# Kernel optimization log

Measured on AMD Instinct MI355X. Metric: run time of the kernel, lower is better.

Reference implementation:

```python
import jax, jax.numpy as jnp
import numpy as np

VOCAB = 32000
D_MODEL = 192
N_LAYERS = 8
D_STATE = 64
EXPAND = 2
D_CONV = 3
NUM_CLASSES = 2
D_INNER = EXPAND * D_MODEL            # 384
DT_RANK = (D_MODEL + 15) // 16        # 12 (mamba_ssm default ceil(d_model/16))
EPS = 1e-6


def rmsnorm(x, w):
    return w * x * jax.lax.rsqrt(jnp.mean(x * x, axis=-1, keepdims=True) + EPS)


def selective_scan(u, dt, A, Bm, Cm):
    # u, dt: (b, T, d_inner); Bm, Cm: (b, T, d_state); A: (d_inner, d_state)
    def step(h, xs):
        dt_t, B_t, C_t, u_t = xs                      # (b,di),(b,ds),(b,ds),(b,di)
        dA = jnp.exp(dt_t[:, :, None] * A)            # (b, di, ds)
        h = dA * h + (dt_t * u_t)[:, :, None] * B_t[:, None, :]
        y = jnp.einsum('bdn,bn->bd', h, C_t)
        return h, y

    b = u.shape[0]
    h0 = jnp.zeros((b, D_INNER, D_STATE), u.dtype)
    xs = (jnp.swapaxes(dt, 0, 1), jnp.swapaxes(Bm, 0, 1),
          jnp.swapaxes(Cm, 0, 1), jnp.swapaxes(u, 0, 1))
    _, ys = jax.lax.scan(step, h0, xs)                # ys: (T, b, di)
    return jnp.swapaxes(ys, 0, 1)


def mamba_layer(x, p):
    # one residual Mamba block: x + Mamba(RMSNorm(x))
    norm_w, in_w, cw, cb, xpw, dtw, dtb, Alog, Dp, ow = p
    h = rmsnorm(x, norm_w)
    xz = jnp.einsum('btd,ed->bte', h, in_w)           # (b, T, 2*di)
    xi, z = jnp.split(xz, 2, axis=-1)
    # causal depthwise conv over time
    xc = jnp.swapaxes(xi, 1, 2)                       # (b, di, T)
    xc = jax.lax.conv_general_dilated(xc, cw[:, None, :], (1,),
                                      [(D_CONV - 1, 0)],
                                      feature_group_count=D_INNER)
    xi = jax.nn.silu(jnp.swapaxes(xc, 1, 2) + cb)
    dbl = jnp.einsum('btc,ec->bte', xi, xpw)          # (b, T, dt_rank+2*ds)
    dt_r = dbl[..., :DT_RANK]
    Bm = dbl[..., DT_RANK:DT_RANK + D_STATE]
    Cm = dbl[..., DT_RANK + D_STATE:]
    dt = jax.nn.softplus(jnp.einsum('btr,dr->btd', dt_r, dtw) + dtb)
    A = -jnp.exp(Alog)
    y = selective_scan(xi, dt, A, Bm, Cm) + xi * Dp
    y = y * jax.nn.silu(z)
    return x + jnp.einsum('bte,de->btd', y, ow)


def setup_inputs():
    key = jax.random.key(0)
    ks = jax.random.split(key, 12)
    B, L = 8, 1024
    s = 0.02
    input_ids = jax.random.randint(ks[0], (B, L), 0, VOCAB, dtype=jnp.int32)
    attention_mask = jnp.ones((B, L), dtype=jnp.int32)
    embed = jax.random.normal(ks[1], (VOCAB, D_MODEL), jnp.float32) * s
    cls = jax.random.normal(ks[2], (1, 1, D_MODEL), jnp.float32) * s
    norm_w = jnp.ones((N_LAYERS, D_MODEL), jnp.float32)
    in_proj_w = jax.random.normal(ks[3], (N_LAYERS, 2 * D_INNER, D_MODEL), jnp.float32) * s
    conv_w = jax.random.normal(ks[4], (N_LAYERS, D_INNER, D_CONV), jnp.float32) * s
    conv_b = jnp.zeros((N_LAYERS, D_INNER), jnp.float32)
    x_proj_w = jax.random.normal(ks[5], (N_LAYERS, DT_RANK + 2 * D_STATE, D_INNER), jnp.float32) * s
    dt_proj_w = jax.random.normal(ks[6], (N_LAYERS, D_INNER, DT_RANK), jnp.float32) * s
    dt_proj_b = jnp.zeros((N_LAYERS, D_INNER), jnp.float32)
    # mamba_ssm S4D-real init: A_log = log(1..d_state)
    A_log = jnp.log(jnp.tile(jnp.arange(1.0, D_STATE + 1, dtype=jnp.float32)[None, None, :],
                             (N_LAYERS, D_INNER, 1)))
    D_param = jnp.ones((N_LAYERS, D_INNER), jnp.float32)
    out_proj_w = jax.random.normal(ks[7], (N_LAYERS, D_MODEL, D_INNER), jnp.float32) * s
    final_norm_w = jnp.ones((D_MODEL,), jnp.float32)
    head_w = embed[:NUM_CLASSES]            # tie_embeddings=True
    head_b = jnp.zeros((NUM_CLASSES,), jnp.float32)
    return dict(input_ids=input_ids, attention_mask=attention_mask, embed=embed,
                cls=cls, norm_w=norm_w, in_proj_w=in_proj_w, conv_w=conv_w,
                conv_b=conv_b, x_proj_w=x_proj_w, dt_proj_w=dt_proj_w,
                dt_proj_b=dt_proj_b, A_log=A_log, D_param=D_param,
                out_proj_w=out_proj_w, final_norm_w=final_norm_w,
                head_w=head_w, head_b=head_b)


def reference(input_ids, attention_mask, embed, cls, norm_w, in_proj_w, conv_w,
              conv_b, x_proj_w, dt_proj_w, dt_proj_b, A_log, D_param,
              out_proj_w, final_norm_w, head_w, head_b):
    x = embed[input_ids]                               # (b, L, d)
    b = x.shape[0]
    x = jnp.concatenate([x, jnp.broadcast_to(cls, (b, 1, D_MODEL))], axis=1)
    layer_fn = jax.checkpoint(mamba_layer)

    def body(x, p):
        return layer_fn(x, p), None

    x, _ = jax.lax.scan(body, x, (norm_w, in_proj_w, conv_w, conv_b, x_proj_w,
                                  dt_proj_w, dt_proj_b, A_log, D_param, out_proj_w))
    x = rmsnorm(x, final_norm_w)
    m = attention_mask.astype(x.dtype)                 # (b, L)
    denom = jnp.clip(jnp.sum(m, axis=1, keepdims=True), 1.0, None)
    pooled = jnp.sum(x[:, :-1] * m[..., None], axis=1) / denom
    return pooled @ head_w.T + head_b                  # (b, num_classes)
```

## Files before the change

kernel.cpp:

```cpp
#include <hip/hip_runtime.h>
#include <hip/hip_bf16.h>
#include <cstddef>

namespace {

constexpr int NB   = 8;
constexpr int LSEQ = 1025;
constexpr int TSEQ = 1024;
constexpr int DM   = 192;
constexpr int DI   = 384;
constexpr int DXZ  = 768;
constexpr int DBLW = 140;
constexpr int DTR  = 12;
constexpr int NST  = 64;
constexpr int MROWS = NB * LSEQ;
constexpr int NCH  = 32;
constexpr int CS   = 32;
constexpr int NCH1 = NCH - 1;
constexpr int NDG  = DI / 64;
constexpr int HST  = 32;
constexpr int XPAD = 144;
constexpr float LOG2E = 1.4426950408889634f;

using bf16x8 = __attribute__((ext_vector_type(8))) short;
using f32x4  = __attribute__((ext_vector_type(4))) float;

__device__ __forceinline__ float waveReduceSum(float v) {
#pragma unroll
  for (int o = 32; o; o >>= 1) v += __shfl_xor(v, o, 64);
  return v;
}

__device__ __forceinline__ unsigned short f2bf(float v) {
  __hip_bfloat16 b = __float2bfloat16(v);
  return *reinterpret_cast<unsigned short*>(&b);
}

__global__ void embed_kernel(const int* __restrict__ ids, const float* __restrict__ emb,
                             const float* __restrict__ cls, float* __restrict__ x) {
  int idx = blockIdx.x * blockDim.x + threadIdx.x;
  if (idx >= NB * LSEQ * DM) return;
  int d = idx % DM;
  int bt = idx / DM;
  int t = bt % LSEQ, b = bt / LSEQ;
  float v;
  if (t < TSEQ) v = emb[(size_t)ids[b * TSEQ + t] * DM + d];
  else          v = cls[d];
  x[idx] = v;
}

__global__ void cvt_bf16_kernel(const float* __restrict__ src, unsigned short* __restrict__ dst,
                                int n) {
  int idx = blockIdx.x * blockDim.x + threadIdx.x;
  if (idx < n) dst[idx] = f2bf(src[idx]);
}

__global__ void pad_xp_kernel(const float* __restrict__ src, unsigned short* __restrict__ dst) {
  int idx = blockIdx.x * blockDim.x + threadIdx.x;
  if (idx >= 8 * XPAD * DI) return;
  int k = idx % DI;
  int n = (idx / DI) % XPAD;
  int l = idx / (DI * XPAD);
  float v = (n < DBLW) ? src[((size_t)l * DBLW + n) * DI + k] : 0.f;
  dst[idx] = f2bf(v);
}

__global__ void transpose_batched(const float* __restrict__ in, float* __restrict__ out,
                                  int rows, int cols) {
  __shared__ float tile[32][33];
  int l = blockIdx.z;
  int r0 = blockIdx.y * 32, c0 = blockIdx.x * 32;
  const float* src = in + (size_t)l * rows * cols;
  float* dst = out + (size_t)l * rows * cols;
  int tx = threadIdx.x, ty = threadIdx.y;
#pragma unroll
  for (int i = 0; i < 32; i += 8) {
    int r = r0 + ty + i, c = c0 + tx;
    if (r < rows && c < cols) tile[ty + i][tx] = src[(size_t)r * cols + c];
  }
  __syncthreads();
#pragma unroll
  for (int i = 0; i < 32; i += 8) {
    int c = c0 + ty + i, r = r0 + tx;
    if (c < cols && r < rows) dst[(size_t)c * rows + r] = tile[tx][ty + i];
  }
}

__global__ __launch_bounds__(192)
void rmsnorm_kernel(const float* __restrict__ x, const float* __restrict__ w,
                    unsigned short* __restrict__ h) {
  int row = blockIdx.x;
  int d = threadIdx.x;
  float v = x[(size_t)row * DM + d];
  float ss = waveReduceSum(v * v);
  __shared__ float red[3];
  if ((d & 63) == 0) red[d >> 6] = ss;
  __syncthreads();
  float ms = (red[0] + red[1] + red[2]) * (1.f / DM);
  h[(size_t)row * DM + d] = f2bf(v * rsqrtf(ms + 1e-6f) * w[d]);
}

template <int EPI, int ASRC>
__global__ __launch_bounds__(256)
void gemm_mfma(const unsigned short* __restrict__ A, const float* __restrict__ A0,
               const float* __restrict__ A1, const unsigned short* __restrict__ W,
               float* __restrict__ C, int M, int Nw, int Nstore, int K, int ldc) {
  __shared__ unsigned short Alds[128][40];
  __shared__ unsigned short Wlds[64][40];
  const int tid = threadIdx.x;
  const int w = tid >> 6, lane = tid & 63;
  const int r16 = lane & 15, g = lane >> 4;
  const int row0 = blockIdx.y * 128, col0 = blockIdx.x * 64;

  f32x4 acc[2][4];
#pragma unroll
  for (int mi = 0; mi < 2; ++mi)
#pragma unroll
    for (int ni = 0; ni < 4; ++ni) acc[mi][ni] = (f32x4){0.f, 0.f, 0.f, 0.f};

  for (int k0 = 0; k0 < K; k0 += 32) {
#pragma unroll
    for (int cc = 0; cc < 2; ++cc) {
      int c = tid + cc * 256;
      int r = c >> 2, q = c & 3;
      uint4 v = make_uint4(0, 0, 0, 0);
      int grow = row0 + r;
      if (grow < M) {
        if (ASRC == 0) {
          v = *(const uint4*)(A + (size_t)grow * K + k0 + q * 8);
        } else {
          const float* s0 = A0 + (size_t)grow * K + k0 + q * 8;
          const float* s1 = A1 + (size_t)grow * K + k0 + q * 8;
          float4 p0 = *(const float4*)s0, p1 = *(const float4*)(s0 + 4);
          float4 q0 = *(const float4*)s1, q1 = *(const float4*)(s1 + 4);
          v.x = (unsigned)f2bf(p0.x + q0.x) | ((unsigned)f2bf(p0.y + q0.y) << 16);
          v.y = (unsigned)f2bf(p0.z + q0.z) | ((unsigned)f2bf(p0.w + q0.w) << 16);
          v.z = (unsigned)f2bf(p1.x + q1.x) | ((unsigned)f2bf(p1.y + q1.y) << 16);
          v.w = (unsigned)f2bf(p1.z + q1.z) | ((unsigned)f2bf(p1.w + q1.w) << 16);
        }
      }
      *(uint4*)&Alds[r][q * 8] = v;
    }
    {
      int r = tid >> 2, q = tid & 3;
      uint4 v = make_uint4(0, 0, 0, 0);
      int gn = col0 + r;
      if (gn < Nw) v = *(const uint4*)(W + (size_t)gn * K + k0 + q * 8);
      *(uint4*)&Wlds[r][q * 8] = v;
    }
    __syncthreads();
    bf16x8 a_f[2], b_f[4];
#pragma unroll
    for (int mi = 0; mi < 2; ++mi)
      a_f[mi] = *(const bf16x8*)&Alds[w * 32 + mi * 16 + r16][g * 8];
#pragma unroll
    for (int ni = 0; ni < 4; ++ni)
      b_f[ni] = *(const bf16x8*)&Wlds[ni * 16 + r16][g * 8];
#pragma unroll
    for (int mi = 0; mi < 2; ++mi)
#pragma unroll
      for (int ni = 0; ni < 4; ++ni)
        acc[mi][ni] = __builtin_amdgcn_mfma_f32_16x16x32_bf16(a_f[mi], b_f[ni],
                                                              acc[mi][ni], 0, 0, 0);
    __syncthreads();
  }
#pragma unroll
  for (int mi = 0; mi < 2; ++mi) {
#pragma unroll
    for (int reg = 0; reg < 4; ++reg) {
      int row = row0 + w * 32 + mi * 16 + g * 4 + reg;
      if (row >= M) continue;
#pragma unroll
      for (int ni = 0; ni < 4; ++ni) {
        int col = col0 + ni * 16 + r16;
        if (col >= Nstore) continue;
        size_t idx = (size_t)row * ldc + col;
        if (EPI) C[idx] += acc[mi][ni][reg];
        else     C[idx] = acc[mi][ni][reg];
      }
    }
  }
}

__global__ void conv_kernel(const float* __restrict__ xz, const float* __restrict__ cw,
                            const float* __restrict__ cb, float* __restrict__ xi,
                            unsigned short* __restrict__ xi16, float* __restrict__ zg) {
  int idx = blockIdx.x * blockDim.x + threadIdx.x;
  if (idx >= NB * LSEQ * DI) return;
  int c = idx % DI;
  int bt = idx / DI;
  int t = bt % LSEQ, b = bt / LSEQ;
  const float* src = xz + (size_t)b * LSEQ * DXZ + c;
  float s = cb[c];
  float w0 = cw[c * 3 + 0], w1 = cw[c * 3 + 1], w2 = cw[c * 3 + 2];
  if (t >= 2) s = fmaf(w0, src[(size_t)(t - 2) * DXZ], s);
  if (t >= 1) s = fmaf(w1, src[(size_t)(t - 1) * DXZ], s);
  s = fmaf(w2, src[(size_t)t * DXZ], s);
  float sig = 1.f / (1.f + __expf(-s));
  float u = s * sig;
  xi[idx] = u;
  xi16[idx] = f2bf(u);
  float zv = src[(size_t)t * DXZ + DI];
  float zsig = 1.f / (1.f + __expf(-zv));
  zg[idx] = zv * zsig;
}

__global__ __launch_bounds__(384)
void dt_kernel(const float* __restrict__ dbl, const float* __restrict__ dtwT,
               const float* __restrict__ dtb, float* __restrict__ dtout) {
  int row0 = blockIdx.x * 4;
  int d = threadIdx.x;
  __shared__ float rr[4][DTR];
  if (d < 4 * DTR) rr[d / DTR][d % DTR] = dbl[(size_t)(row0 + d / DTR) * DBLW + (d % DTR)];
  float w[DTR];
#pragma unroll
  for (int r = 0; r < DTR; ++r) w[r] = dtwT[r * DI + d];
  float bias = dtb[d];
  __syncthreads();
#pragma unroll
  for (int q = 0; q < 4; ++q) {
    float s = bias;
#pragma unroll
    for (int r = 0; r < DTR; ++r) s = fmaf(rr[q][r], w[r], s);
    float sp = fmaxf(s, 0.f) + log1pf(__expf(-fabsf(s)));
    dtout[(size_t)(row0 + q) * DI + d] = sp;
  }
}


__global__ __launch_bounds__(256, 3)
void scan_pass1(const float* __restrict__ dtp_, const float* __restrict__ xi,
                const float* __restrict__ dbl, const float* __restrict__ Alog,
                float* __restrict__ cumdt, float* __restrict__ H) {
  __shared__ float Bt[2][CS][64];
  const int tid = threadIdx.x;
  const int wid = tid >> 6, lane = tid & 63;
  const int q = wid >> 1, half = wid & 1;
  const int unit = blockIdx.x * 2 + q;
  const int c = unit % NCH1;
  const int bg = unit / NCH1;
  const int b = bg / NDG, dgrp = bg % NDG;
  const int d = dgrp * 64 + lane;
  const int n0 = half * HST;
  const int t0 = c * CS;

  {
    const float* srcB = dbl + ((size_t)b * LSEQ + t0) * DBLW + DTR + lane;
    for (int r = half; r < CS; r += 2) Bt[q][r][lane] = srcB[(size_t)r * DBLW];
  }

  const float* Ap = Alog + (size_t)d * NST;
  float a0 = __expf(Ap[0]);
  bool okl = true;
#pragma unroll
  for (int j = 0; j < HST; ++j) {
    float aj = __expf(Ap[n0 + j]);
    okl = okl && (fabsf(aj - (float)(n0 + j + 1) * a0) <= 1e-3f * (float)(n0 + j + 1) * fabsf(a0));
  }
  const bool fast = __all(okl);
  const float al2u = -a0 * LOG2E;

  float h[HST];
#pragma unroll
  for (int j = 0; j < HST; ++j) h[j] = 0.f;

  __syncthreads();

  const float* dtp = dtp_ + ((size_t)b * LSEQ + t0) * DI + d;
  const float* up  = xi   + ((size_t)b * LSEQ + t0) * DI + d;
  float cum = 0.f;
  float dtv = *dtp, uv = *up;

  if (fast) {
    for (int t = 0; t < CS; ++t) {
      float n_dt = 0.f, n_u = 0.f;
      if (t + 1 < CS) {
        dtp += DI; up += DI;
        n_dt = *dtp; n_u = *up;
      }
      float dtu = dtv * uv;
      float m = dtv * al2u;
      float r1 = exp2f(m);
      float p = (n0 == 0) ? r1 : exp2f(m * (float)(n0 + 1));
      float r2 = r1 * r1, r4 = r2 * r2;
      float s0 = p, s1 = p * r1, s2 = p * r2, s3 = s2 * r1;
#pragma unroll
      for (int k = 0; k < 8; ++k) {
        float4 B4 = *(const float4*)&Bt[q][t][n0 + 4 * k];
        h[4 * k + 0] = fmaf(s0, h[4 * k + 0], dtu * B4.x);
        h[4 * k + 1] = fmaf(s1, h[4 * k + 1], dtu * B4.y);
        h[4 * k + 2] = fmaf(s2, h[4 * k + 2], dtu * B4.z);
        h[4 * k + 3] = fmaf(s3, h[4 * k + 3], dtu * B4.w);
        if (k < 7) { s0 *= r4; s1 *= r4; s2 *= r4; s3 *= r4; }
      }
      cum += dtv;
      dtv = n_dt; uv = n_u;
    }
  } else {
    for (int t = 0; t < CS; ++t) {
      float n_dt = 0.f, n_u = 0.f;
      if (t + 1 < CS) {
        dtp += DI; up += DI;
        n_dt = *dtp; n_u = *up;
      }
      float dtu = dtv * uv;
      for (int j = 0; j < HST; ++j) {
        float aj = -__expf(Ap[n0 + j]) * LOG2E;
        h[j] = fmaf(exp2f(dtv * aj), h[j], dtu * Bt[q][t][n0 + j]);
      }
      cum += dtv;
      dtv = n_dt; uv = n_u;
    }
  }

  if (half == 0)
    cumdt[(size_t)bg * NCH1 * 64 + (size_t)c * 64 + lane] = cum;
  float* hp = H + ((size_t)bg * NCH + (c + 1)) * NST * 64 + (size_t)n0 * 64 + lane;
#pragma unroll
  for (int j = 0; j < HST; ++j) hp[j * 64] = h[j];
}

__global__ __launch_bounds__(256)
void scan_pass2(const float* __restrict__ cumdt, const float* __restrict__ Alog,
                float* __restrict__ H) {
  int gw = blockIdx.x * 4 + (threadIdx.x >> 6);
  int lane = threadIdx.x & 63;
  int bg = gw >> 4;
  int nq = (gw & 15) * 4;
  int dgrp = bg % NDG;
  int d = dgrp * 64 + lane;

  float al2[4];
#pragma unroll
  for (int j = 0; j < 4; ++j) al2[j] = -__expf(Alog[(size_t)d * NST + nq + j]) * LOG2E;

  float h[4] = {0.f, 0.f, 0.f, 0.f};

  float* H0 = H + ((size_t)bg * NCH) * NST * 64 + (size_t)nq * 64 + lane;
#pragma unroll
  for (int j = 0; j < 4; ++j) H0[j * 64] = 0.f;

  for (int c = 1; c < NCH; ++c) {
    float cum = cumdt[(size_t)bg * NCH1 * 64 + (size_t)(c - 1) * 64 + lane];
    float* Hc = H + ((size_t)bg * NCH + c) * NST * 64 + (size_t)nq * 64 + lane;
#pragma unroll
    for (int j = 0; j < 4; ++j) {
      float he = Hc[j * 64];
      h[j] = fmaf(exp2f(al2[j] * cum), h[j], he);
      Hc[j * 64] = h[j];
    }
  }
}

__global__ __launch_bounds__(256, 3)
void scan_pass3(const float* __restrict__ dtp_, const float* __restrict__ xi,
                const float* __restrict__ zg, const float* __restrict__ dbl,
                const float* __restrict__ Alog, const float* __restrict__ Dpar,
                const float* __restrict__ H, float* __restrict__ yg0,
                float* __restrict__ yg1) {
  __shared__ float Bt[2][CS + 1][64];
  __shared__ float Ct[2][CS + 1][64];
  const int tid = threadIdx.x;
  const int wid = tid >> 6, lane = tid & 63;
  const int q = wid >> 1, half = wid & 1;
  const int unit = blockIdx.x * 2 + q;
  const int c = unit & (NCH - 1);
  const int bg = unit >> 5;
  const int b = bg / NDG, dgrp = bg % NDG;
  const int d = dgrp * 64 + lane;
  const int n0 = half * HST;
  const int t0 = c * CS;
  const int nsteps = (c == NCH - 1) ? (LSEQ - t0) : CS;

  {
    const float* srcB = dbl + ((size_t)b * LSEQ + t0) * DBLW + DTR + (half ? NST : 0) + lane;
    float* dst = half ? &Ct[q][0][lane] : &Bt[q][0][lane];
    for (int r = 0; r < nsteps; ++r) dst[r * 64] = srcB[(size_t)r * DBLW];
  }

  const float* Ap = Alog + (size_t)d * NST;
  float a0 = __expf(Ap[0]);
  bool okl = true;
#pragma unroll
  for (int j = 0; j < HST; ++j) {
    float aj = __expf(Ap[n0 + j]);
    okl = okl && (fabsf(aj - (float)(n0 + j + 1) * a0) <= 1e-3f * (float)(n0 + j + 1) * fabsf(a0));
  }
  const bool fast = __all(okl);
  const float al2u = -a0 * LOG2E;

  float Dp = Dpar[d];
  float h[HST];
  {
    const float* hi = H + ((size_t)bg * NCH + c) * NST * 64 + (size_t)n0 * 64 + lane;
#pragma unroll
    for (int j = 0; j < HST; ++j) h[j] = hi[j * 64];
  }

  __syncthreads();

  const float* dtp = dtp_ + ((size_t)b * LSEQ + t0) * DI + d;
  const float* up  = xi   + ((size_t)b * LSEQ + t0) * DI + d;
  const float* gp  = zg   + ((size_t)b * LSEQ + t0) * DI + d;
  float* yp = (half == 0 ? yg0 : yg1) + ((size_t)b * LSEQ + t0) * DI + d;

  float dtv = *dtp, uv = *up, gv = *gp;

  if (fast) {
    for (int t = 0; t < nsteps; ++t) {
      float n_dt = 0.f, n_u = 0.f, n_g = 0.f;
      if (t + 1 < nsteps) {
        dtp += DI; up += DI; gp += DI;
        n_dt = *dtp; n_u = *up; n_g = *gp;
      }
      float dtu = dtv * uv;
      float m = dtv * al2u;
      float r1 = exp2f(m);
      float p = (n0 == 0) ? r1 : exp2f(m * (float)(n0 + 1));
      float r2 = r1 * r1, r4 = r2 * r2;
      float s0 = p, s1 = p * r1, s2 = p * r2, s3 = s2 * r1;
      float y = 0.f;
#pragma unroll
      for (int k = 0; k < 8; ++k) {
        float4 B4 = *(const float4*)&Bt[q][t][n0 + 4 * k];
        float4 C4 = *(const float4*)&Ct[q][t][n0 + 4 * k];
        h[4 * k + 0] = fmaf(s0, h[4 * k + 0], dtu * B4.x);
        y = fmaf(h[4 * k + 0], C4.x, y);
        h[4 * k + 1] = fmaf(s1, h[4 * k + 1], dtu * B4.y);
        y = fmaf(h[4 * k + 1], C4.y, y);
        h[4 * k + 2] = fmaf(s2, h[4 * k + 2], dtu * B4.z);
        y = fmaf(h[4 * k + 2], C4.z, y);
        h[4 * k + 3] = fmaf(s3, h[4 * k + 3], dtu * B4.w);
        y = fmaf(h[4 * k + 3], C4.w, y);
        if (k < 7) { s0 *= r4; s1 *= r4; s2 *= r4; s3 *= r4; }
      }
      float outv = (half == 0) ? fmaf(uv, Dp, y) * gv : y * gv;
      *yp = outv;
      yp += DI;
      dtv = n_dt; uv = n_u; gv = n_g;
    }
  } else {
    for (int t = 0; t < nsteps; ++t) {
      float n_dt = 0.f, n_u = 0.f, n_g = 0.f;
      if (t + 1 < nsteps) {
        dtp += DI; up += DI; gp += DI;
        n_dt = *dtp; n_u = *up; n_g = *gp;
      }
      float dtu = dtv * uv;
      float y = 0.f;
      for (int j = 0; j < HST; ++j) {
        float aj = -__expf(Ap[n0 + j]) * LOG2E;
        h[j] = fmaf(exp2f(dtv * aj), h[j], dtu * Bt[q][t][n0 + j]);
        y = fmaf(h[j], Ct[q][t][n0 + j], y);
      }
      float outv = (half == 0) ? fmaf(uv, Dp, y) * gv : y * gv;
      *yp = outv;
      yp += DI;
      dtv = n_dt; uv = n_u; gv = n_g;
    }
  }
}

__global__ __launch_bounds__(192)
void pool1_kernel(const float* __restrict__ x, const int* __restrict__ mask,
                  const float* __restrict__ fw, float* __restrict__ partial) {
  int b = blockIdx.x >> 6;
  int chunk = blockIdx.x & 63;
  int d = threadIdx.x;
  __shared__ float red[3];
  float w = fw[d];
  float acc = 0.f;
  for (int tt = 0; tt < 16; ++tt) {
    int t = chunk * 16 + tt;
    float v = x[((size_t)b * LSEQ + t) * DM + d];
    float ss = waveReduceSum(v * v);
    if ((d & 63) == 0) red[d >> 6] = ss;
    __syncthreads();
    float ms = (red[0] + red[1] + red[2]) * (1.f / DM);
    float m = (float)mask[b * TSEQ + t];
    acc = fmaf(v * rsqrtf(ms + 1e-6f) * w, m, acc);
    __syncthreads();
  }
  partial[((size_t)b * 64 + chunk) * DM + d] = acc;
}

__global__ __launch_bounds__(192)
void pool2_kernel(const float* __restrict__ partial, const int* __restrict__ mask,
                  const float* __restrict__ hw, const float* __restrict__ hb,
                  float* __restrict__ out) {
  int b = blockIdx.x;
  int d = threadIdx.x;
  float s = 0.f;
  for (int c = 0; c < 64; ++c) s += partial[((size_t)b * 64 + c) * DM + d];
  float den = 0.f;
  for (int t = d; t < TSEQ; t += DM) den += (float)mask[b * TSEQ + t];
  den = waveReduceSum(den);
  __shared__ float dred[3];
  __shared__ float pooled[DM];
  if ((d & 63) == 0) dred[d >> 6] = den;
  __syncthreads();
  float denom = fmaxf(dred[0] + dred[1] + dred[2], 1.f);
  pooled[d] = s / denom;
  __syncthreads();
  if (d < 2) {
    float acc = hb[d];
    for (int k = 0; k < DM; ++k) acc = fmaf(pooled[k], hw[d * DM + k], acc);
    out[b * 2 + d] = acc;
  }
}

}

extern "C" void kernel_launch(void* const* d_in, const int* in_sizes, int n_in,
                              void* d_out, int out_size, void* d_ws, size_t ws_size,
                              hipStream_t stream) {
  const int*   ids    = (const int*)d_in[0];
  const int*   mask   = (const int*)d_in[1];
  const float* embed  = (const float*)d_in[2];
  const float* cls    = (const float*)d_in[3];
  const float* norm_w = (const float*)d_in[4];
  const float* in_w   = (const float*)d_in[5];
  const float* conv_w = (const float*)d_in[6];
  const float* conv_b = (const float*)d_in[7];
  const float* xp_w   = (const float*)d_in[8];
  const float* dtw    = (const float*)d_in[9];
  const float* dtb    = (const float*)d_in[10];
  const float* Alog   = (const float*)d_in[11];
  const float* Dpar   = (const float*)d_in[12];
  const float* ow     = (const float*)d_in[13];
  const float* fnw    = (const float*)d_in[14];
  const float* hw     = (const float*)d_in[15];
  const float* hb     = (const float*)d_in[16];
  float* out = (float*)d_out;

  char* base = (char*)d_ws;
  size_t off = 0;
  auto alloc = [&](size_t bytes) -> void* {
    void* p = base + off;
    off = (off + bytes + 255) & ~(size_t)255;
    return p;
  };

  float* x      = (float*)alloc((size_t)NB * LSEQ * DM * 4);
  unsigned short* h16 = (unsigned short*)alloc((size_t)NB * LSEQ * DM * 2);
  float* xz     = (float*)alloc((size_t)NB * LSEQ * DXZ * 4);
  float* xi     = (float*)alloc((size_t)NB * LSEQ * DI * 4);
  unsigned short* xi16 = (unsigned short*)alloc((size_t)NB * LSEQ * DI * 2);
  float* zgbuf  = (float*)alloc((size_t)NB * LSEQ * DI * 4);
  float* dblb   = (float*)alloc((size_t)NB * LSEQ * DBLW * 4);
  float* dtbuf  = (float*)alloc((size_t)NB * LSEQ * DI * 4);
  float* yg0    = (float*)alloc((size_t)NB * LSEQ * DI * 4);
  float* yg1    = (float*)alloc((size_t)NB * LSEQ * DI * 4);
  unsigned short* wb_in = (unsigned short*)alloc((size_t)8 * DXZ * DM * 2);
  unsigned short* wb_xp = (unsigned short*)alloc((size_t)8 * XPAD * DI * 2);
  unsigned short* wb_ow = (unsigned short*)alloc((size_t)8 * DM * DI * 2);
  float* wT_dt  = (float*)alloc((size_t)8 * DTR * DI * 4);
  float* partial = (float*)alloc((size_t)NB * 64 * DM * 4);
  float* cumdt  = (float*)alloc((size_t)NB * NDG * NCH1 * 64 * 4);
  float* Hbuf   = (float*)alloc((size_t)NB * NDG * NCH * NST * 64 * 4);

  cvt_bf16_kernel<<<(8 * DXZ * DM + 255) / 256, 256, 0, stream>>>(in_w, wb_in, 8 * DXZ * DM);
  pad_xp_kernel<<<(8 * XPAD * DI + 255) / 256, 256, 0, stream>>>(xp_w, wb_xp);
  cvt_bf16_kernel<<<(8 * DM * DI + 255) / 256, 256, 0, stream>>>(ow, wb_ow, 8 * DM * DI);
  dim3 tb(32, 8);
  transpose_batched<<<dim3(1, 12, 8), tb, 0, stream>>>(dtw, wT_dt, DI, DTR);

  embed_kernel<<<(NB * LSEQ * DM) / 256, 256, 0, stream>>>(ids, embed, cls, x);

  const int mtiles = (MROWS + 127) / 128;
  for (int l = 0; l < 8; ++l) {
    rmsnorm_kernel<<<MROWS, 192, 0, stream>>>(x, norm_w + l * DM, h16);
    gemm_mfma<0, 0><<<dim3(DXZ / 64, mtiles), 256, 0, stream>>>(
        h16, nullptr, nullptr, wb_in + (size_t)l * DXZ * DM, xz, MROWS, DXZ, DXZ, DM, DXZ);
    conv_kernel<<<(NB * LSEQ * DI) / 256, 256, 0, stream>>>(
        xz, conv_w + l * DI * 3, conv_b + l * DI, xi, xi16, zgbuf);
    gemm_mfma<0, 0><<<dim3(XPAD / 64 + 1, mtiles), 256, 0, stream>>>(
        xi16, nullptr, nullptr, wb_xp + (size_t)l * XPAD * DI, dblb, MROWS, XPAD, DBLW, DI, DBLW);
    dt_kernel<<<MROWS / 4, DI, 0, stream>>>(dblb, wT_dt + l * DTR * DI, dtb + l * DI, dtbuf);
    scan_pass1<<<(NB * NDG * NCH1) / 2, 256, 0, stream>>>(
        dtbuf, xi, dblb, Alog + (size_t)l * DI * NST, cumdt, Hbuf);
    scan_pass2<<<(NB * NDG * 16) / 4, 256, 0, stream>>>(
        cumdt, Alog + (size_t)l * DI * NST, Hbuf);
    scan_pass3<<<(NB * NDG * NCH) / 2, 256, 0, stream>>>(
        dtbuf, xi, zgbuf, dblb, Alog + (size_t)l * DI * NST, Dpar + l * DI, Hbuf,
        yg0, yg1);
    gemm_mfma<1, 1><<<dim3(DM / 64, mtiles), 256, 0, stream>>>(
        nullptr, yg0, yg1, wb_ow + (size_t)l * DM * DI, x, MROWS, DM, DM, DI, DM);
  }

  pool1_kernel<<<NB * 64, 192, 0, stream>>>(x, mask, fnw, partial);
  pool2_kernel<<<NB, 192, 0, stream>>>(partial, mask, hw, hb, out);
}
```

Measured before the change: 1.265 ms.

## Store xz and scan outputs in bf16, widen scan blocks to share B/C tiles

The in_proj GEMM now writes xz as bf16, and the conv kernel reads it back as bf16. The scan pass3 outputs yg0/yg1 are also stored as bf16 and summed pairwise in bf16 before the out_proj GEMM. This cuts global memory traffic for these intermediates roughly in half. Scan pass1 and pass3 are regrouped into 768-thread blocks covering all six d-groups of one (batch, chunk), so the B/C tiles are loaded into LDS once per block instead of once per d-group. The risks are extra bf16 rounding error in the intermediates and lower occupancy from the larger blocks.

```diff
diff --git a/kernel.cpp b/kernel.cpp
--- a/kernel.cpp
+++ b/kernel.cpp
@@ -35,6 +35,14 @@
   __hip_bfloat16 b = __float2bfloat16(v);
   return *reinterpret_cast<unsigned short*>(&b);
 }
+__device__ __forceinline__ float bf2f(unsigned short u) {
+  return __uint_as_float(((unsigned)u) << 16);
+}
+__device__ __forceinline__ unsigned addpair_bf(unsigned a, unsigned b) {
+  float alo = __uint_as_float(a << 16), ahi = __uint_as_float(a & 0xffff0000u);
+  float blo = __uint_as_float(b << 16), bhi = __uint_as_float(b & 0xffff0000u);
+  return ((unsigned)f2bf(alo + blo)) | (((unsigned)f2bf(ahi + bhi)) << 16);
+}
 
 __global__ void embed_kernel(const int* __restrict__ ids, const float* __restrict__ emb,
                              const float* __restrict__ cls, float* __restrict__ x) {
@@ -102,9 +110,10 @@
 
 template <int EPI, int ASRC>
 __global__ __launch_bounds__(256)
-void gemm_mfma(const unsigned short* __restrict__ A, const float* __restrict__ A0,
-               const float* __restrict__ A1, const unsigned short* __restrict__ W,
-               float* __restrict__ C, int M, int Nw, int Nstore, int K, int ldc) {
+void gemm_mfma(const unsigned short* __restrict__ A, const unsigned short* __restrict__ Ab0,
+               const unsigned short* __restrict__ Ab1, const unsigned short* __restrict__ W,
+               float* __restrict__ C, unsigned short* __restrict__ Cb,
+               int M, int Nw, int Nstore, int K, int ldc) {
   __shared__ unsigned short Alds[128][40];
   __shared__ unsigned short Wlds[64][40];
   const int tid = threadIdx.x;
@@ -129,14 +138,12 @@
         if (ASRC == 0) {
           v = *(const uint4*)(A + (size_t)grow * K + k0 + q * 8);
         } else {
-          const float* s0 = A0 + (size_t)grow * K + k0 + q * 8;
-          const float* s1 = A1 + (size_t)grow * K + k0 + q * 8;
-          float4 p0 = *(const float4*)s0, p1 = *(const float4*)(s0 + 4);
-          float4 q0 = *(const float4*)s1, q1 = *(const float4*)(s1 + 4);
-          v.x = (unsigned)f2bf(p0.x + q0.x) | ((unsigned)f2bf(p0.y + q0.y) << 16);
-          v.y = (unsigned)f2bf(p0.z + q0.z) | ((unsigned)f2bf(p0.w + q0.w) << 16);
-          v.z = (unsigned)f2bf(p1.x + q1.x) | ((unsigned)f2bf(p1.y + q1.y) << 16);
-          v.w = (unsigned)f2bf(p1.z + q1.z) | ((unsigned)f2bf(p1.w + q1.w) << 16);
+          uint4 a = *(const uint4*)(Ab0 + (size_t)grow * K + k0 + q * 8);
+          uint4 b = *(const uint4*)(Ab1 + (size_t)grow * K + k0 + q * 8);
+          v.x = addpair_bf(a.x, b.x);
+          v.y = addpair_bf(a.y, b.y);
+          v.z = addpair_bf(a.z, b.z);
+          v.w = addpair_bf(a.w, b.w);
         }
       }
       *(uint4*)&Alds[r][q * 8] = v;
@@ -175,14 +182,15 @@
         int col = col0 + ni * 16 + r16;
         if (col >= Nstore) continue;
         size_t idx = (size_t)row * ldc + col;
-        if (EPI) C[idx] += acc[mi][ni][reg];
-        else     C[idx] = acc[mi][ni][reg];
-      }
-    }
-  }
-}
-
-__global__ void conv_kernel(const float* __restrict__ xz, const float* __restrict__ cw,
+        if (EPI == 1)      C[idx] += acc[mi][ni][reg];
+        else if (EPI == 0) C[idx] = acc[mi][ni][reg];
+        else               Cb[idx] = f2bf(acc[mi][ni][reg]);
+      }
+    }
+  }
+}
+
+__global__ void conv_kernel(const unsigned short* __restrict__ xz16, const float* __restrict__ cw,
                             const float* __restrict__ cb, float* __restrict__ xi,
                             unsigned short* __restrict__ xi16, float* __restrict__ zg) {
   int idx = blockIdx.x * blockDim.x + threadIdx.x;
@@ -190,17 +198,17 @@
   int c = idx % DI;
   int bt = idx / DI;
   int t = bt % LSEQ, b = bt / LSEQ;
-  const float* src = xz + (size_t)b * LSEQ * DXZ + c;
+  const unsigned short* src = xz16 + (size_t)b * LSEQ * DXZ + c;
   float s = cb[c];
   float w0 = cw[c * 3 + 0], w1 = cw[c * 3 + 1], w2 = cw[c * 3 + 2];
-  if (t >= 2) s = fmaf(w0, src[(size_t)(t - 2) * DXZ], s);
-  if (t >= 1) s = fmaf(w1, src[(size_t)(t - 1) * DXZ], s);
-  s = fmaf(w2, src[(size_t)t * DXZ], s);
+  if (t >= 2) s = fmaf(w0, bf2f(src[(size_t)(t - 2) * DXZ]), s);
+  if (t >= 1) s = fmaf(w1, bf2f(src[(size_t)(t - 1) * DXZ]), s);
+  s = fmaf(w2, bf2f(src[(size_t)t * DXZ]), s);
   float sig = 1.f / (1.f + __expf(-s));
   float u = s * sig;
   xi[idx] = u;
   xi16[idx] = f2bf(u);
-  float zv = src[(size_t)t * DXZ + DI];
+  float zv = bf2f(src[(size_t)t * DXZ + DI]);
   float zsig = 1.f / (1.f + __expf(-zv));
   zg[idx] = zv * zsig;
 }
@@ -228,25 +236,24 @@
 }
 
 
-__global__ __launch_bounds__(256, 3)
+__global__ __launch_bounds__(768, 3)
 void scan_pass1(const float* __restrict__ dtp_, const float* __restrict__ xi,
                 const float* __restrict__ dbl, const float* __restrict__ Alog,
                 float* __restrict__ cumdt, float* __restrict__ H) {
-  __shared__ float Bt[2][CS][64];
+  __shared__ float Bt[CS][64];
   const int tid = threadIdx.x;
-  const int wid = tid >> 6, lane = tid & 63;
-  const int q = wid >> 1, half = wid & 1;
-  const int unit = blockIdx.x * 2 + q;
-  const int c = unit % NCH1;
-  const int bg = unit / NCH1;
-  const int b = bg / NDG, dgrp = bg % NDG;
+  const int w = tid >> 6, lane = tid & 63;
+  const int dgrp = w >> 1, half = w & 1;
+  const int b = blockIdx.x / NCH1;
+  const int c = blockIdx.x % NCH1;
+  const int bg = b * NDG + dgrp;
   const int d = dgrp * 64 + lane;
   const int n0 = half * HST;
   const int t0 = c * CS;
 
   {
     const float* srcB = dbl + ((size_t)b * LSEQ + t0) * DBLW + DTR + lane;
-    for (int r = half; r < CS; r += 2) Bt[q][r][lane] = srcB[(size_t)r * DBLW];
+    for (int r = w; r < CS; r += 12) Bt[r][lane] = srcB[(size_t)r * DBLW];
   }
 
   const float* Ap = Alog + (size_t)d * NST;
@@ -286,7 +293,7 @@
       float s0 = p, s1 = p * r1, s2 = p * r2, s3 = s2 * r1;
 #pragma unroll
       for (int k = 0; k < 8; ++k) {
-        float4 B4 = *(const float4*)&Bt[q][t][n0 + 4 * k];
+        float4 B4 = *(const float4*)&Bt[t][n0 + 4 * k];
         h[4 * k + 0] = fmaf(s0, h[4 * k + 0], dtu * B4.x);
         h[4 * k + 1] = fmaf(s1, h[4 * k + 1], dtu * B4.y);
         h[4 * k + 2] = fmaf(s2, h[4 * k + 2], dtu * B4.z);
@@ -306,7 +313,7 @@
       float dtu = dtv * uv;
       for (int j = 0; j < HST; ++j) {
         float aj = -__expf(Ap[n0 + j]) * LOG2E;
-        h[j] = fmaf(exp2f(dtv * aj), h[j], dtu * Bt[q][t][n0 + j]);
+        h[j] = fmaf(exp2f(dtv * aj), h[j], dtu * Bt[t][n0 + j]);
       }
       cum += dtv;
       dtv = n_dt; uv = n_u;
@@ -352,30 +359,33 @@
   }
 }
 
-__global__ __launch_bounds__(256, 3)
+__global__ __launch_bounds__(768, 3)
 void scan_pass3(const float* __restrict__ dtp_, const float* __restrict__ xi,
                 const float* __restrict__ zg, const float* __restrict__ dbl,
                 const float* __restrict__ Alog, const float* __restrict__ Dpar,
-                const float* __restrict__ H, float* __restrict__ yg0,
-                float* __restrict__ yg1) {
-  __shared__ float Bt[2][CS + 1][64];
-  __shared__ float Ct[2][CS + 1][64];
+                const float* __restrict__ H, unsigned short* __restrict__ yb0,
+                unsigned short* __restrict__ yb1) {
+  __shared__ float Bt[CS + 1][64];
+  __shared__ float Ct[CS + 1][64];
   const int tid = threadIdx.x;
-  const int wid = tid >> 6, lane = tid & 63;
-  const int q = wid >> 1, half = wid & 1;
-  const int unit = blockIdx.x * 2 + q;
-  const int c = unit & (NCH - 1);
-  const int bg = unit >> 5;
-  const int b = bg / NDG, dgrp = bg % NDG;
+  const int w = tid >> 6, lane = tid & 63;
+  const int dgrp = w >> 1, half = w & 1;
+  const int b = blockIdx.x >> 5;
+  const int c = blockIdx.x & 31;
+  const int bg = b * NDG + dgrp;
   const int d = dgrp * 64 + lane;
   const int n0 = half * HST;
   const int t0 = c * CS;
   const int nsteps = (c == NCH - 1) ? (LSEQ - t0) : CS;
 
   {
-    const float* srcB = dbl + ((size_t)b * LSEQ + t0) * DBLW + DTR + (half ? NST : 0) + lane;
-    float* dst = half ? &Ct[q][0][lane] : &Bt[q][0][lane];
-    for (int r = 0; r < nsteps; ++r) dst[r * 64] = srcB[(size_t)r * DBLW];
+    if (w < 6) {
+      const float* srcB = dbl + ((size_t)b * LSEQ + t0) * DBLW + DTR + lane;
+      for (int r = w; r < nsteps; r += 6) Bt[r][lane] = srcB[(size_t)r * DBLW];
+    } else {
+      const float* srcC = dbl + ((size_t)b * LSEQ + t0) * DBLW + DTR + NST + lane;
+      for (int r = w - 6; r < nsteps; r += 6) Ct[r][lane] = srcC[(size_t)r * DBLW];
+    }
   }
 
   const float* Ap = Alog + (size_t)d * NST;
@@ -402,7 +412,7 @@
   const float* dtp = dtp_ + ((size_t)b * LSEQ + t0) * DI + d;
   const float* up  = xi   + ((size_t)b * LSEQ + t0) * DI + d;
   const float* gp  = zg   + ((size_t)b * LSEQ + t0) * DI + d;
-  float* yp = (half == 0 ? yg0 : yg1) + ((size_t)b * LSEQ + t0) * DI + d;
+  unsigned short* yp = (half == 0 ? yb0 : yb1) + ((size_t)b * LSEQ + t0) * DI + d;
 
   float dtv = *dtp, uv = *up, gv = *gp;
 
@@ -422,8 +432,8 @@
       float y = 0.f;
 #pragma unroll
       for (int k = 0; k < 8; ++k) {
-        float4 B4 = *(const float4*)&Bt[q][t][n0 + 4 * k];
-        float4 C4 = *(const float4*)&Ct[q][t][n0 + 4 * k];
+        float4 B4 = *(const float4*)&Bt[t][n0 + 4 * k];
+        float4 C4 = *(const float4*)&Ct[t][n0 + 4 * k];
         h[4 * k + 0] = fmaf(s0, h[4 * k + 0], dtu * B4.x);
         y = fmaf(h[4 * k + 0], C4.x, y);
         h[4 * k + 1] = fmaf(s1, h[4 * k + 1], dtu * B4.y);
@@ -435,7 +445,7 @@
         if (k < 7) { s0 *= r4; s1 *= r4; s2 *= r4; s3 *= r4; }
       }
       float outv = (half == 0) ? fmaf(uv, Dp, y) * gv : y * gv;
-      *yp = outv;
+      *yp = f2bf(outv);
       yp += DI;
       dtv = n_dt; uv = n_u; gv = n_g;
     }
@@ -450,11 +460,11 @@
       float y = 0.f;
       for (int j = 0; j < HST; ++j) {
         float aj = -__expf(Ap[n0 + j]) * LOG2E;
-        h[j] = fmaf(exp2f(dtv * aj), h[j], dtu * Bt[q][t][n0 + j]);
-        y = fmaf(h[j], Ct[q][t][n0 + j], y);
+        h[j] = fmaf(exp2f(dtv * aj), h[j], dtu * Bt[t][n0 + j]);
+        y = fmaf(h[j], Ct[t][n0 + j], y);
       }
       float outv = (half == 0) ? fmaf(uv, Dp, y) * gv : y * gv;
-      *yp = outv;
+      *yp = f2bf(outv);
       yp += DI;
       dtv = n_dt; uv = n_u; gv = n_g;
     }
@@ -543,14 +553,14 @@
 
   float* x      = (float*)alloc((size_t)NB * LSEQ * DM * 4);
   unsigned short* h16 = (unsigned short*)alloc((size_t)NB * LSEQ * DM * 2);
-  float* xz     = (float*)alloc((size_t)NB * LSEQ * DXZ * 4);
+  unsigned short* xz16 = (unsigned short*)alloc((size_t)NB * LSEQ * DXZ * 2);
   float* xi     = (float*)alloc((size_t)NB * LSEQ * DI * 4);
   unsigned short* xi16 = (unsigned short*)alloc((size_t)NB * LSEQ * DI * 2);
   float* zgbuf  = (float*)alloc((size_t)NB * LSEQ * DI * 4);
   float* dblb   = (float*)alloc((size_t)NB * LSEQ * DBLW * 4);
   float* dtbuf  = (float*)alloc((size_t)NB * LSEQ * DI * 4);
-  float* yg0    = (float*)alloc((size_t)NB * LSEQ * DI * 4);
-  float* yg1    = (float*)alloc((size_t)NB * LSEQ * DI * 4);
+  unsigned short* yb0 = (unsigned short*)alloc((size_t)NB * LSEQ * DI * 2);
+  unsigned short* yb1 = (unsigned short*)alloc((size_t)NB * LSEQ * DI * 2);
   unsigned short* wb_in = (unsigned short*)alloc((size_t)8 * DXZ * DM * 2);
   unsigned short* wb_xp = (unsigned short*)alloc((size_t)8 * XPAD * DI * 2);
   unsigned short* wb_ow = (unsigned short*)alloc((size_t)8 * DM * DI * 2);
@@ -570,22 +580,25 @@
   const int mtiles = (MROWS + 127) / 128;
   for (int l = 0; l < 8; ++l) {
     rmsnorm_kernel<<<MROWS, 192, 0, stream>>>(x, norm_w + l * DM, h16);
-    gemm_mfma<0, 0><<<dim3(DXZ / 64, mtiles), 256, 0, stream>>>(
-        h16, nullptr, nullptr, wb_in + (size_t)l * DXZ * DM, xz, MROWS, DXZ, DXZ, DM, DXZ);
+    gemm_mfma<2, 0><<<dim3(DXZ / 64, mtiles), 256, 0, stream>>>(
+        h16, nullptr, nullptr, wb_in + (size_t)l * DXZ * DM, nullptr, xz16,
+        MROWS, DXZ, DXZ, DM, DXZ);
     conv_kernel<<<(NB * LSEQ * DI) / 256, 256, 0, stream>>>(
-        xz, conv_w + l * DI * 3, conv_b + l * DI, xi, xi16, zgbuf);
+        xz16, conv_w + l * DI * 3, conv_b + l * DI, xi, xi16, zgbuf);
     gemm_mfma<0, 0><<<dim3(XPAD / 64 + 1, mtiles), 256, 0, stream>>>(
-        xi16, nullptr, nullptr, wb_xp + (size_t)l * XPAD * DI, dblb, MROWS, XPAD, DBLW, DI, DBLW);
+        xi16, nullptr, nullptr, wb_xp + (size_t)l * XPAD * DI, dblb, nullptr,
+        MROWS, XPAD, DBLW, DI, DBLW);
     dt_kernel<<<MROWS / 4, DI, 0, stream>>>(dblb, wT_dt + l * DTR * DI, dtb + l * DI, dtbuf);
-    scan_pass1<<<(NB * NDG * NCH1) / 2, 256, 0, stream>>>(
+    scan_pass1<<<NB * NCH1, 768, 0, stream>>>(
         dtbuf, xi, dblb, Alog + (size_t)l * DI * NST, cumdt, Hbuf);
     scan_pass2<<<(NB * NDG * 16) / 4, 256, 0, stream>>>(
         cumdt, Alog + (size_t)l * DI * NST, Hbuf);
-    scan_pass3<<<(NB * NDG * NCH) / 2, 256, 0, stream>>>(
+    scan_pass3<<<NB * NCH, 768, 0, stream>>>(
         dtbuf, xi, zgbuf, dblb, Alog + (size_t)l * DI * NST, Dpar + l * DI, Hbuf,
-        yg0, yg1);
+        yb0, yb1);
     gemm_mfma<1, 1><<<dim3(DM / 64, mtiles), 256, 0, stream>>>(
-        nullptr, yg0, yg1, wb_ow + (size_t)l * DM * DI, x, MROWS, DM, DM, DI, DM);
+        nullptr, yb0, yb1, wb_ow + (size_t)l * DM * DI, x, nullptr,
+        MROWS, DM, DM, DI, DM);
   }
 
   pool1_kernel<<<NB * 64, 192, 0, stream>>>(x, mask, fnw, partial);
```

After: 1.261 ms. Within noise of the previous version (-0.3%).
